# Kernel tuning notes

Measured on AMD Instinct MI355X. Metric: run time of the kernel, lower is better.

Reference implementation:

```python
import jax, jax.numpy as jnp
import numpy as np

N_HEAD = 16

def setup_inputs() -> dict:
    key = jax.random.key(0)
    ks = jax.random.split(key, 5)
    B, S, C = 4, 2048, 1024
    x = jax.random.normal(ks[0], (B, S, C), dtype=jnp.float32)
    w_qkv = jax.random.normal(ks[1], (C, 3 * C), dtype=jnp.float32) * (1.0 / np.sqrt(C))
    b_qkv = jnp.zeros((3 * C,), dtype=jnp.float32)
    w_proj = jax.random.normal(ks[2], (C, C), dtype=jnp.float32) * (1.0 / np.sqrt(C))
    b_proj = jnp.zeros((C,), dtype=jnp.float32)
    return {"x": x, "w_qkv": w_qkv, "b_qkv": b_qkv, "w_proj": w_proj, "b_proj": b_proj}

def reference(x, w_qkv, b_qkv, w_proj, b_proj):
    B, S, C = x.shape
    H = N_HEAD
    D = C // H
    qkv = x @ w_qkv + b_qkv                       # [B,S,3C]
    q, k, v = jnp.split(qkv, 3, axis=-1)
    # [B,S,C] -> [B,H,S,D]
    q = q.reshape(B, S, H, D).transpose(0, 2, 1, 3)
    k = k.reshape(B, S, H, D).transpose(0, 2, 1, 3)
    v = v.reshape(B, S, H, D).transpose(0, 2, 1, 3)
    scores = jnp.einsum('bhqd,bhkd->bhqk', q, k) / jnp.sqrt(jnp.float32(D))
    causal = jnp.tril(jnp.ones((S, S), dtype=bool))
    scores = jnp.where(causal[None, None], scores, -jnp.inf)
    weights = jax.nn.softmax(scores, axis=-1)     # dropout p=0 -> identity
    out = jnp.einsum('bhqk,bhkd->bhqd', weights, v)
    out = out.transpose(0, 2, 1, 3).reshape(B, S, C)
    return out @ w_proj + b_proj
```

## Files before the change

### kernel.cpp

```cpp
#include <hip/hip_runtime.h>

#define SDIM 2048
#define CDIM 1024
#define BDIM 4
#define HDIM 16
#define DDIM 64

#define ATT_SCALE 0.18033688011112042f

typedef __attribute__((ext_vector_type(8))) short bf16x8;
typedef __attribute__((ext_vector_type(4))) short bf16x4;
typedef __attribute__((ext_vector_type(4))) float f32x4;
typedef unsigned short u16;

#define MFMA __builtin_amdgcn_mfma_f32_16x16x32_bf16
#define LDS_ORDER_FENCE() __asm__ __volatile__("" ::: "memory")

__device__ __forceinline__ u16 f2b(float f) {
    union { float f; unsigned u; } v; v.f = f;
    unsigned r = v.u + 0x7FFFu + ((v.u >> 16) & 1u);
    return (u16)(r >> 16);
}
__device__ __forceinline__ u16 f2b_trunc(float f) {
    union { float f; unsigned u; } v; v.f = f;
    return (u16)(v.u >> 16);
}

typedef const __attribute__((address_space(1))) unsigned int* gas_t;
typedef __attribute__((address_space(3))) unsigned int* las_t;
__device__ __forceinline__ void cp16(const void* g, void* l) {
    __builtin_amdgcn_global_load_lds((gas_t)g, (las_t)l, 16, 0, 0);
}

__device__ __forceinline__ float fast_exp2(float x) {
#if __has_builtin(__builtin_amdgcn_exp2f)
    return __builtin_amdgcn_exp2f(x);
#else
    return __exp2f(x);
#endif
}

__global__ __launch_bounds__(256) void prep(
    const float* __restrict__ x, const float* __restrict__ w_qkv,
    const float* __restrict__ w_proj,
    u16* __restrict__ Xb, u16* __restrict__ WqT, u16* __restrict__ WpT)
{
    __shared__ __align__(16) u16 t[64][72];
    const int bx = blockIdx.x;
    const int tid = threadIdx.x;

    if (bx < 4096) {
        int i = (bx * 256 + tid) * 8;
        float4 a = *reinterpret_cast<const float4*>(&x[i]);
        float4 b = *reinterpret_cast<const float4*>(&x[i + 4]);
        u16 u[8];
        u[0]=f2b(a.x); u[1]=f2b(a.y); u[2]=f2b(a.z); u[3]=f2b(a.w);
        u[4]=f2b(b.x); u[5]=f2b(b.y); u[6]=f2b(b.z); u[7]=f2b(b.w);
        *reinterpret_cast<uint4*>(&Xb[i]) = *reinterpret_cast<uint4*>(u);
        return;
    }

    const float* src; u16* dst; int N, n0, k0;
    if (bx < 4096 + 768) {
        int b2 = bx - 4096;
        src = w_qkv; dst = WqT; N = 3 * CDIM;
        n0 = (b2 % 48) * 64; k0 = (b2 / 48) * 64;
    } else {
        int b2 = bx - 4864;
        src = w_proj; dst = WpT; N = CDIM;
        n0 = (b2 % 16) * 64; k0 = (b2 / 16) * 64;
    }
    const int K = CDIM;
#pragma unroll
    for (int it = 0; it < 4; it++) {
        int c = tid + it * 256;
        int r = c >> 4, c4 = (c & 15) * 4;
        float4 f = *reinterpret_cast<const float4*>(&src[(size_t)(k0 + r) * N + n0 + c4]);
        t[c4 + 0][r] = f2b(f.x);
        t[c4 + 1][r] = f2b(f.y);
        t[c4 + 2][r] = f2b(f.z);
        t[c4 + 3][r] = f2b(f.w);
    }
    __syncthreads();
#pragma unroll
    for (int it = 0; it < 2; it++) {
        int c = tid + it * 256;
        int r = c >> 3, c8 = (c & 7) * 8;
        *reinterpret_cast<uint4*>(&dst[(size_t)(n0 + r) * K + k0 + c8]) =
            *reinterpret_cast<const uint4*>(&t[r][c8]);
    }
}

__global__ __launch_bounds__(256, 4) void gemm_qkv(
    const u16* __restrict__ A, const u16* __restrict__ Bt,
    const float* __restrict__ bias,
    u16* __restrict__ Qb, u16* __restrict__ Kb, u16* __restrict__ Vtb)
{
    __shared__ __align__(16) u16 As[128 * 64];
    __shared__ __align__(16) u16 Bs[128 * 64];
    __shared__ __align__(16) u16 Eb[4][16 * 68];
    const int tid = threadIdx.x, lane = tid & 63, wave = tid >> 6;
    const int wm = wave >> 1, wn = wave & 1;
    const int l16 = lane & 15, quad = lane >> 4;
    const int m0 = blockIdx.y * 128, n0 = blockIdx.x * 128;
    const int K = CDIM;

    const int l8 = lane & 7, lr = lane >> 3;
    const int sg = l8 ^ lr;

    f32x4 acc[4][4];
#pragma unroll
    for (int i = 0; i < 4; i++)
#pragma unroll
        for (int j = 0; j < 4; j++) acc[i][j] = (f32x4){0.f, 0.f, 0.f, 0.f};

    for (int k0 = 0; k0 < K; k0 += 64) {
        __syncthreads();
#pragma unroll
        for (int u = 0; u < 4; u++) {
            int row = wave * 32 + u * 8 + lr;
            cp16(&A [(size_t)(m0 + row) * K + k0 + sg * 8], &As[(wave * 4 + u) * 512]);
            cp16(&Bt[(size_t)(n0 + row) * K + k0 + sg * 8], &Bs[(wave * 4 + u) * 512]);
        }
        __syncthreads();

#pragma unroll
        for (int kk = 0; kk < 2; kk++) {
            bf16x8 a[4], b[4];
#pragma unroll
            for (int i = 0; i < 4; i++) {
                int row = wm * 64 + i * 16 + l16;
                a[i] = *reinterpret_cast<const bf16x8*>(
                    &As[(row * 8 + ((kk * 4 + quad) ^ (l16 & 7))) * 8]);
            }
#pragma unroll
            for (int j = 0; j < 4; j++) {
                int row = wn * 64 + j * 16 + l16;
                b[j] = *reinterpret_cast<const bf16x8*>(
                    &Bs[(row * 8 + ((kk * 4 + quad) ^ (l16 & 7))) * 8]);
            }
#pragma unroll
            for (int i = 0; i < 4; i++)
#pragma unroll
                for (int j = 0; j < 4; j++)
                    acc[i][j] = MFMA(a[i], b[j], acc[i][j], 0, 0, 0);
        }
    }

    const int mm0 = m0 + wm * 64;
    const int bidx = mm0 >> 11, s0 = mm0 & 2047;
    const int n_base = n0 + wn * 64;
    u16* eb = &Eb[wave][0];
    const int erow = lane >> 2, ec = (lane & 3) * 16;

    if (n0 >= 2 * CDIM) {
        const int h = (n_base - 2 * CDIM) >> 6;
        const size_t gb = ((size_t)(bidx * HDIM + h)) * DDIM * SDIM;
#pragma unroll
        for (int j = 0; j < 4; j++) {
            float bvj = bias[n_base + j * 16 + l16];
            LDS_ORDER_FENCE();
#pragma unroll
            for (int i = 0; i < 4; i++)
#pragma unroll
                for (int r = 0; r < 4; r++)
                    eb[l16 * 68 + i * 16 + quad * 4 + r] = f2b(acc[i][j][r] + bvj);
            LDS_ORDER_FENCE();
            union { bf16x4 hp[4]; uint4 u[2]; } pk;
            pk.hp[0] = *reinterpret_cast<const bf16x4*>(&eb[erow * 68 + ec]);
            pk.hp[1] = *reinterpret_cast<const bf16x4*>(&eb[erow * 68 + ec + 4]);
            pk.hp[2] = *reinterpret_cast<const bf16x4*>(&eb[erow * 68 + ec + 8]);
            pk.hp[3] = *reinterpret_cast<const bf16x4*>(&eb[erow * 68 + ec + 12]);
            u16* gp = &Vtb[gb + (size_t)(j * 16 + erow) * SDIM + s0 + ec];
            *reinterpret_cast<uint4*>(gp)     = pk.u[0];
            *reinterpret_cast<uint4*>(gp + 8) = pk.u[1];
        }
    } else {
        const bool isK = (n_base >= CDIM);
        u16* dst = isK ? Kb : Qb;
        const float scale = isK ? 1.0f : ATT_SCALE;
        const int hh = (n_base & 1023) >> 6;
        const size_t hb = ((size_t)(bidx * HDIM + hh)) * SDIM;
        float bvj[4];
#pragma unroll
        for (int j = 0; j < 4; j++) bvj[j] = bias[n_base + j * 16 + l16];
#pragma unroll
        for (int i = 0; i < 4; i++) {
            LDS_ORDER_FENCE();
#pragma unroll
            for (int j = 0; j < 4; j++)
#pragma unroll
                for (int r = 0; r < 4; r++)
                    eb[(quad * 4 + r) * 68 + j * 16 + l16] =
                        f2b((acc[i][j][r] + bvj[j]) * scale);
            LDS_ORDER_FENCE();
            union { bf16x4 hp[4]; uint4 u[2]; } pk;
            pk.hp[0] = *reinterpret_cast<const bf16x4*>(&eb[erow * 68 + ec]);
            pk.hp[1] = *reinterpret_cast<const bf16x4*>(&eb[erow * 68 + ec + 4]);
            pk.hp[2] = *reinterpret_cast<const bf16x4*>(&eb[erow * 68 + ec + 8]);
            pk.hp[3] = *reinterpret_cast<const bf16x4*>(&eb[erow * 68 + ec + 12]);
            const int s = s0 + i * 16 + erow;
            u16* gp = &dst[(hb + s) * DDIM + ec];
            *reinterpret_cast<uint4*>(gp)     = pk.u[0];
            *reinterpret_cast<uint4*>(gp + 8) = pk.u[1];
        }
    }
}

__global__ __launch_bounds__(512, 6) void attn(
    const u16* __restrict__ Qb, const u16* __restrict__ Kb,
    const u16* __restrict__ Vtb, u16* __restrict__ Ob)
{
    __shared__ __align__(16) u16 Ks[2][64 * 64];
    __shared__ __align__(16) u16 Vts[2][64 * 64];
    __shared__ __align__(16) u16 Ps[8][16 * 68];

    const int tid = threadIdx.x;
    const int lane = tid & 63, wave = tid >> 6;
    const int l16 = lane & 15, quad = lane >> 4;
    const int x = blockIdx.x;
    const int bh = (x & 7) * 8 + ((x >> 3) & 7);
    const int qt = 15 - (x >> 6);
    const int q0 = qt * 128;
    const int b = bh >> 4, h = bh & 15;
    const size_t base = (size_t)bh * (SDIM * DDIM);

    const int cl0 = wave * 64 + lane;
    const int sr0 = cl0 >> 3, scc = cl0 & 7;
    const int sg0 = scc ^ (sr0 & 7);

    const int qrow = q0 + wave * 16 + l16;
    bf16x8 aq0 = *reinterpret_cast<const bf16x8*>(&Qb[base + (size_t)qrow * DDIM + quad * 8]);
    bf16x8 aq1 = *reinterpret_cast<const bf16x8*>(&Qb[base + (size_t)qrow * DDIM + 32 + quad * 8]);

    u16* Pw = &Ps[wave][0];

    f32x4 O[4];
    f32x4 Osum = (f32x4){0.f, 0.f, 0.f, 0.f};
#pragma unroll
    for (int j = 0; j < 4; j++) O[j] = (f32x4){0.f, 0.f, 0.f, 0.f};
    const short onev = (l16 == 0) ? (short)0x3F80 : (short)0;
    const bf16x8 bones = {onev, onev, onev, onev, onev, onev, onev, onev};

    const int nkb = (qt + 1) * 2;
    const int Arow = q0 + wave * 16;

    cp16(&Kb [base + (size_t)sr0 * DDIM + sg0 * 8], &Ks[0][wave * 512]);
    cp16(&Vtb[base + (size_t)sr0 * SDIM + sg0 * 8], &Vts[0][wave * 512]);

    for (int kbi = 0; kbi < nkb; kbi++) {
        const int cur = kbi & 1;
        const int kb = kbi * 64;
        __syncthreads();
        if (kbi + 1 < nkb) {
            const int kb2 = kb + 64;
            cp16(&Kb [base + (size_t)(kb2 + sr0) * DDIM + sg0 * 8], &Ks[1 - cur][wave * 512]);
            cp16(&Vtb[base + (size_t)sr0 * SDIM + kb2 + sg0 * 8], &Vts[1 - cur][wave * 512]);
        }
        if (kb > Arow + 15) continue;

        const u16* Kc = &Ks[cur][0];
        const u16* Vc = &Vts[cur][0];

        f32x4 sc[4];
#pragma unroll
        for (int j = 0; j < 4; j++) {
            int kr = j * 16 + l16;
            bf16x8 bk0 = *reinterpret_cast<const bf16x8*>(&Kc[(kr * 8 + ( quad      ^ (kr & 7))) * 8]);
            bf16x8 bk1 = *reinterpret_cast<const bf16x8*>(&Kc[(kr * 8 + ((quad + 4) ^ (kr & 7))) * 8]);
            f32x4 s = (f32x4){0.f, 0.f, 0.f, 0.f};
            s = MFMA(aq0, bk0, s, 0, 0, 0);
            s = MFMA(aq1, bk1, s, 0, 0, 0);
            sc[j] = s;
        }
        if (kb + 63 > Arow) {
            const int qrel = Arow - kb;
#pragma unroll
            for (int j = 0; j < 4; j++) {
                int kk = j * 16 + l16;
#pragma unroll
                for (int r = 0; r < 4; r++)
                    sc[j][r] = (kk <= qrel + quad * 4 + r) ? sc[j][r] : -1e30f;
            }
        }
#pragma unroll
        for (int j = 0; j < 4; j++)
#pragma unroll
            for (int r = 0; r < 4; r++) {
                float p = fast_exp2(sc[j][r]);
                Pw[(quad * 4 + r) * 68 + j * 16 + l16] = f2b_trunc(p);
            }
        LDS_ORDER_FENCE();
        union { bf16x4 hp[2]; bf16x8 f; } a0u, a1u;
        a0u.hp[0] = *reinterpret_cast<const bf16x4*>(&Pw[l16 * 68 + quad * 8]);
        a0u.hp[1] = *reinterpret_cast<const bf16x4*>(&Pw[l16 * 68 + quad * 8 + 4]);
        a1u.hp[0] = *reinterpret_cast<const bf16x4*>(&Pw[l16 * 68 + 32 + quad * 8]);
        a1u.hp[1] = *reinterpret_cast<const bf16x4*>(&Pw[l16 * 68 + 32 + quad * 8 + 4]);

#pragma unroll
        for (int j = 0; j < 4; j++) {
            int vr = j * 16 + l16;
            bf16x8 bv0 = *reinterpret_cast<const bf16x8*>(&Vc[(vr * 8 + ( quad      ^ (vr & 7))) * 8]);
            bf16x8 bv1 = *reinterpret_cast<const bf16x8*>(&Vc[(vr * 8 + ((quad + 4) ^ (vr & 7))) * 8]);
            O[j] = MFMA(a0u.f, bv0, O[j], 0, 0, 0);
            O[j] = MFMA(a1u.f, bv1, O[j], 0, 0, 0);
        }
        Osum = MFMA(a0u.f, bones, Osum, 0, 0, 0);
        Osum = MFMA(a1u.f, bones, Osum, 0, 0, 0);
    }

#pragma unroll
    for (int r = 0; r < 4; r++) {
        float l = __shfl(Osum[r], (lane & 48));
        float inv = 1.0f / l;
        int s = q0 + wave * 16 + quad * 4 + r;
#pragma unroll
        for (int j = 0; j < 4; j++)
            Ob[((size_t)(b * SDIM + s)) * CDIM + h * 64 + j * 16 + l16] =
                f2b(O[j][r] * inv);
    }
}

__global__ __launch_bounds__(256, 4) void gemm_proj(
    const u16* __restrict__ A, const u16* __restrict__ Bt,
    const float* __restrict__ bias, float* __restrict__ out)
{
    __shared__ __align__(16) u16 As[128 * 64];
    __shared__ __align__(16) u16 Bs[128 * 64];
    const int tid = threadIdx.x, lane = tid & 63, wave = tid >> 6;
    const int wm = wave >> 1, wn = wave & 1;
    const int l16 = lane & 15, quad = lane >> 4;
    const int m0 = blockIdx.y * 128, n0 = blockIdx.x * 128;
    const int K = CDIM, N = CDIM;

    const int l8 = lane & 7, lr = lane >> 3;
    const int sg = l8 ^ lr;

    f32x4 acc[4][4];
#pragma unroll
    for (int i = 0; i < 4; i++)
#pragma unroll
        for (int j = 0; j < 4; j++) acc[i][j] = (f32x4){0.f, 0.f, 0.f, 0.f};

    for (int k0 = 0; k0 < K; k0 += 64) {
        __syncthreads();
#pragma unroll
        for (int u = 0; u < 4; u++) {
            int row = wave * 32 + u * 8 + lr;
            cp16(&A [(size_t)(m0 + row) * K + k0 + sg * 8], &As[(wave * 4 + u) * 512]);
            cp16(&Bt[(size_t)(n0 + row) * K + k0 + sg * 8], &Bs[(wave * 4 + u) * 512]);
        }
        __syncthreads();

#pragma unroll
        for (int kk = 0; kk < 2; kk++) {
            bf16x8 a[4], b[4];
#pragma unroll
            for (int i = 0; i < 4; i++) {
                int row = wm * 64 + i * 16 + l16;
                a[i] = *reinterpret_cast<const bf16x8*>(
                    &As[(row * 8 + ((kk * 4 + quad) ^ (l16 & 7))) * 8]);
            }
#pragma unroll
            for (int j = 0; j < 4; j++) {
                int row = wn * 64 + j * 16 + l16;
                b[j] = *reinterpret_cast<const bf16x8*>(
                    &Bs[(row * 8 + ((kk * 4 + quad) ^ (l16 & 7))) * 8]);
            }
#pragma unroll
            for (int i = 0; i < 4; i++)
#pragma unroll
                for (int j = 0; j < 4; j++)
                    acc[i][j] = MFMA(a[i], b[j], acc[i][j], 0, 0, 0);
        }
    }

#pragma unroll
    for (int i = 0; i < 4; i++) {
        int mbase = m0 + wm * 64 + i * 16 + quad * 4;
#pragma unroll
        for (int j = 0; j < 4; j++) {
            int n = n0 + wn * 64 + j * 16 + l16;
            float bv = bias[n];
#pragma unroll
            for (int r = 0; r < 4; r++)
                out[(size_t)(mbase + r) * N + n] = acc[i][j][r] + bv;
        }
    }
}

extern "C" void kernel_launch(void* const* d_in, const int* in_sizes, int n_in,
                              void* d_out, int out_size, void* d_ws, size_t ws_size,
                              hipStream_t stream) {
    const float* x      = (const float*)d_in[0];
    const float* w_qkv  = (const float*)d_in[1];
    const float* b_qkv  = (const float*)d_in[2];
    const float* w_proj = (const float*)d_in[3];
    const float* b_proj = (const float*)d_in[4];
    float* out = (float*)d_out;

    const size_t per = (size_t)BDIM * HDIM * SDIM * DDIM;
    u16* Qb  = (u16*)d_ws;
    u16* Kb  = Qb + per;
    u16* Vtb = Kb + per;
    u16* Ob  = Vtb + per;
    u16* Xb  = Ob;
    u16* WqT = Ob + per;
    u16* WpT = WqT + (size_t)3 * CDIM * CDIM;

    dim3 blk(256);
    prep<<<dim3(4096 + 768 + 256), blk, 0, stream>>>(x, w_qkv, w_proj, Xb, WqT, WpT);

    gemm_qkv<<<dim3(3 * CDIM / 128, BDIM * SDIM / 128), blk, 0, stream>>>(
        Xb, WqT, b_qkv, Qb, Kb, Vtb);
    attn<<<dim3(BDIM * HDIM * (SDIM / 128)), dim3(512), 0, stream>>>(Qb, Kb, Vtb, Ob);
    gemm_proj<<<dim3(CDIM / 128, BDIM * SDIM / 128), blk, 0, stream>>>(
        Ob, WpT, b_proj, out);
}
```

Before: 244.9 us.

## Double-buffer GEMM tiles with 256x128 blocks, 8 waves, and XCD-aware block swizzle

Both projection GEMMs now use 512-thread blocks computing 256x128 tiles with double-buffered LDS. The next K tile is prefetched while the current one feeds MFMAs, and the loop waits with partial vmcnt and raw barriers. This aims to overlap global loads with compute and halve the number of B-tile loads per output. Block IDs are remapped across the 8 XCDs for better L2 locality, and s_setprio is raised around the MFMA bursts. The cost is more LDS per block (about 96KB), which lowers occupancy, and the hand-written waitcnt logic is fragile.

```diff
diff --git a/kernel.cpp b/kernel.cpp
--- a/kernel.cpp
+++ b/kernel.cpp
@@ -91,38 +91,61 @@
     }
 }
 
-__global__ __launch_bounds__(256, 4) void gemm_qkv(
+__global__ __launch_bounds__(512, 2) void gemm_qkv(
     const u16* __restrict__ A, const u16* __restrict__ Bt,
     const float* __restrict__ bias,
     u16* __restrict__ Qb, u16* __restrict__ Kb, u16* __restrict__ Vtb)
 {
-    __shared__ __align__(16) u16 As[128 * 64];
-    __shared__ __align__(16) u16 Bs[128 * 64];
-    __shared__ __align__(16) u16 Eb[4][16 * 68];
+    __shared__ __align__(16) u16 As[2][256 * 64];
+    __shared__ __align__(16) u16 Bs[2][128 * 64];
+    __shared__ __align__(16) u16 Eb[8][16 * 68];
     const int tid = threadIdx.x, lane = tid & 63, wave = tid >> 6;
     const int wm = wave >> 1, wn = wave & 1;
     const int l16 = lane & 15, quad = lane >> 4;
-    const int m0 = blockIdx.y * 128, n0 = blockIdx.x * 128;
+    const int bid = blockIdx.x;
+    const int w = (bid & 7) * 96 + (bid >> 3);
+    const int bx = w % 24, by = w / 24;
+    const int m0 = by * 256, n0 = bx * 128;
     const int K = CDIM;
 
     const int l8 = lane & 7, lr = lane >> 3;
     const int sg = l8 ^ lr;
 
+#define STAGE_QKV(buf, k0)                                                    \
+    {                                                                         \
+        _Pragma("unroll")                                                     \
+        for (int s = 0; s < 4; s++) {                                         \
+            int row = s * 64 + wave * 8 + lr;                                 \
+            cp16(&A[(size_t)(m0 + row) * K + (k0) + sg * 8],                  \
+                 &As[buf][(s * 512 + wave * 64) * 8]);                        \
+        }                                                                     \
+        _Pragma("unroll")                                                     \
+        for (int s = 0; s < 2; s++) {                                         \
+            int row = s * 64 + wave * 8 + lr;                                 \
+            cp16(&Bt[(size_t)(n0 + row) * K + (k0) + sg * 8],                 \
+                 &Bs[buf][(s * 512 + wave * 64) * 8]);                        \
+        }                                                                     \
+    }
+
     f32x4 acc[4][4];
 #pragma unroll
     for (int i = 0; i < 4; i++)
 #pragma unroll
         for (int j = 0; j < 4; j++) acc[i][j] = (f32x4){0.f, 0.f, 0.f, 0.f};
 
-    for (int k0 = 0; k0 < K; k0 += 64) {
-        __syncthreads();
-#pragma unroll
-        for (int u = 0; u < 4; u++) {
-            int row = wave * 32 + u * 8 + lr;
-            cp16(&A [(size_t)(m0 + row) * K + k0 + sg * 8], &As[(wave * 4 + u) * 512]);
-            cp16(&Bt[(size_t)(n0 + row) * K + k0 + sg * 8], &Bs[(wave * 4 + u) * 512]);
-        }
-        __syncthreads();
+    const int NT = K / 64;
+    STAGE_QKV(0, 0);
+
+    for (int t = 0; t < NT; t++) {
+        const int cur = t & 1;
+        if (t + 1 < NT) {
+            STAGE_QKV(cur ^ 1, (t + 1) * 64);
+            __asm__ __volatile__("s_waitcnt vmcnt(6)" ::: "memory");
+        } else {
+            __asm__ __volatile__("s_waitcnt vmcnt(0)" ::: "memory");
+        }
+        __builtin_amdgcn_s_barrier();
+        LDS_ORDER_FENCE();
 
 #pragma unroll
         for (int kk = 0; kk < 2; kk++) {
@@ -131,21 +154,27 @@
             for (int i = 0; i < 4; i++) {
                 int row = wm * 64 + i * 16 + l16;
                 a[i] = *reinterpret_cast<const bf16x8*>(
-                    &As[(row * 8 + ((kk * 4 + quad) ^ (l16 & 7))) * 8]);
+                    &As[cur][(row * 8 + ((kk * 4 + quad) ^ (l16 & 7))) * 8]);
             }
 #pragma unroll
             for (int j = 0; j < 4; j++) {
                 int row = wn * 64 + j * 16 + l16;
                 b[j] = *reinterpret_cast<const bf16x8*>(
-                    &Bs[(row * 8 + ((kk * 4 + quad) ^ (l16 & 7))) * 8]);
-            }
+                    &Bs[cur][(row * 8 + ((kk * 4 + quad) ^ (l16 & 7))) * 8]);
+            }
+            __builtin_amdgcn_s_setprio(1);
 #pragma unroll
             for (int i = 0; i < 4; i++)
 #pragma unroll
                 for (int j = 0; j < 4; j++)
                     acc[i][j] = MFMA(a[i], b[j], acc[i][j], 0, 0, 0);
-        }
-    }
+            __builtin_amdgcn_s_setprio(0);
+        }
+        __asm__ __volatile__("s_waitcnt lgkmcnt(0)" ::: "memory");
+        __builtin_amdgcn_s_barrier();
+        LDS_ORDER_FENCE();
+    }
+#undef STAGE_QKV
 
     const int mm0 = m0 + wm * 64;
     const int bidx = mm0 >> 11, s0 = mm0 & 2047;
@@ -321,36 +350,59 @@
     }
 }
 
-__global__ __launch_bounds__(256, 4) void gemm_proj(
+__global__ __launch_bounds__(512, 2) void gemm_proj(
     const u16* __restrict__ A, const u16* __restrict__ Bt,
     const float* __restrict__ bias, float* __restrict__ out)
 {
-    __shared__ __align__(16) u16 As[128 * 64];
-    __shared__ __align__(16) u16 Bs[128 * 64];
+    __shared__ __align__(16) u16 As[2][256 * 64];
+    __shared__ __align__(16) u16 Bs[2][128 * 64];
     const int tid = threadIdx.x, lane = tid & 63, wave = tid >> 6;
     const int wm = wave >> 1, wn = wave & 1;
     const int l16 = lane & 15, quad = lane >> 4;
-    const int m0 = blockIdx.y * 128, n0 = blockIdx.x * 128;
+    const int bid = blockIdx.x;
+    const int w = (bid & 7) * 32 + (bid >> 3);
+    const int bx = w & 7, by = w >> 3;
+    const int m0 = by * 256, n0 = bx * 128;
     const int K = CDIM, N = CDIM;
 
     const int l8 = lane & 7, lr = lane >> 3;
     const int sg = l8 ^ lr;
 
+#define STAGE_PROJ(buf, k0)                                                   \
+    {                                                                         \
+        _Pragma("unroll")                                                     \
+        for (int s = 0; s < 4; s++) {                                         \
+            int row = s * 64 + wave * 8 + lr;                                 \
+            cp16(&A[(size_t)(m0 + row) * K + (k0) + sg * 8],                  \
+                 &As[buf][(s * 512 + wave * 64) * 8]);                        \
+        }                                                                     \
+        _Pragma("unroll")                                                     \
+        for (int s = 0; s < 2; s++) {                                         \
+            int row = s * 64 + wave * 8 + lr;                                 \
+            cp16(&Bt[(size_t)(n0 + row) * K + (k0) + sg * 8],                 \
+                 &Bs[buf][(s * 512 + wave * 64) * 8]);                        \
+        }                                                                     \
+    }
+
     f32x4 acc[4][4];
 #pragma unroll
     for (int i = 0; i < 4; i++)
 #pragma unroll
         for (int j = 0; j < 4; j++) acc[i][j] = (f32x4){0.f, 0.f, 0.f, 0.f};
 
-    for (int k0 = 0; k0 < K; k0 += 64) {
-        __syncthreads();
-#pragma unroll
-        for (int u = 0; u < 4; u++) {
-            int row = wave * 32 + u * 8 + lr;
-            cp16(&A [(size_t)(m0 + row) * K + k0 + sg * 8], &As[(wave * 4 + u) * 512]);
-            cp16(&Bt[(size_t)(n0 + row) * K + k0 + sg * 8], &Bs[(wave * 4 + u) * 512]);
-        }
-        __syncthreads();
+    const int NT = K / 64;
+    STAGE_PROJ(0, 0);
+
+    for (int t = 0; t < NT; t++) {
+        const int cur = t & 1;
+        if (t + 1 < NT) {
+            STAGE_PROJ(cur ^ 1, (t + 1) * 64);
+            __asm__ __volatile__("s_waitcnt vmcnt(6)" ::: "memory");
+        } else {
+            __asm__ __volatile__("s_waitcnt vmcnt(0)" ::: "memory");
+        }
+        __builtin_amdgcn_s_barrier();
+        LDS_ORDER_FENCE();
 
 #pragma unroll
         for (int kk = 0; kk < 2; kk++) {
@@ -359,21 +411,27 @@
             for (int i = 0; i < 4; i++) {
                 int row = wm * 64 + i * 16 + l16;
                 a[i] = *reinterpret_cast<const bf16x8*>(
-                    &As[(row * 8 + ((kk * 4 + quad) ^ (l16 & 7))) * 8]);
+                    &As[cur][(row * 8 + ((kk * 4 + quad) ^ (l16 & 7))) * 8]);
             }
 #pragma unroll
             for (int j = 0; j < 4; j++) {
                 int row = wn * 64 + j * 16 + l16;
                 b[j] = *reinterpret_cast<const bf16x8*>(
-                    &Bs[(row * 8 + ((kk * 4 + quad) ^ (l16 & 7))) * 8]);
-            }
+                    &Bs[cur][(row * 8 + ((kk * 4 + quad) ^ (l16 & 7))) * 8]);
+            }
+            __builtin_amdgcn_s_setprio(1);
 #pragma unroll
             for (int i = 0; i < 4; i++)
 #pragma unroll
                 for (int j = 0; j < 4; j++)
                     acc[i][j] = MFMA(a[i], b[j], acc[i][j], 0, 0, 0);
-        }
-    }
+            __builtin_amdgcn_s_setprio(0);
+        }
+        __asm__ __volatile__("s_waitcnt lgkmcnt(0)" ::: "memory");
+        __builtin_amdgcn_s_barrier();
+        LDS_ORDER_FENCE();
+    }
+#undef STAGE_PROJ
 
 #pragma unroll
     for (int i = 0; i < 4; i++) {
@@ -408,12 +466,9 @@
     u16* WqT = Ob + per;
     u16* WpT = WqT + (size_t)3 * CDIM * CDIM;
 
-    dim3 blk(256);
-    prep<<<dim3(4096 + 768 + 256), blk, 0, stream>>>(x, w_qkv, w_proj, Xb, WqT, WpT);
-
-    gemm_qkv<<<dim3(3 * CDIM / 128, BDIM * SDIM / 128), blk, 0, stream>>>(
-        Xb, WqT, b_qkv, Qb, Kb, Vtb);
+    prep<<<dim3(4096 + 768 + 256), dim3(256), 0, stream>>>(x, w_qkv, w_proj, Xb, WqT, WpT);
+
+    gemm_qkv<<<dim3(768), dim3(512), 0, stream>>>(Xb, WqT, b_qkv, Qb, Kb, Vtb);
     attn<<<dim3(BDIM * HDIM * (SDIM / 128)), dim3(512), 0, stream>>>(Qb, Kb, Vtb, Ob);
-    gemm_proj<<<dim3(CDIM / 128, BDIM * SDIM / 128), blk, 0, stream>>>(
-        Ob, WpT, b_proj, out);
-}
+    gemm_proj<<<dim3(256), dim3(512), 0, stream>>>(Ob, WpT, b_proj, out);
+}
```

New measurement: 251.7 us. +2.8%, slower.
